# Performance work log

Hardware: AMD Instinct MI355X
Metric: run time of the kernel (lower is better)

The kernel has to match this reference:

```python
import jax, jax.numpy as jnp
import numpy as np

B, N, M, L = 4, 2048, 64, 64  # batch, targets, neighbors, lr_dim


def setup_inputs() -> dict:
    key = jax.random.key(0)
    ks = jax.random.split(key, 7)
    return {
        "targets_receptor": jax.random.normal(ks[0], (B, N, L), dtype=jnp.float32),
        "neighbors_ligand": jax.random.normal(ks[1], (B, N, M, L), dtype=jnp.float32),
        "a": jax.random.uniform(ks[2], (B, N, M), dtype=jnp.float32),
        "kernel_l": jax.random.normal(ks[3], (1, 1, L), dtype=jnp.float32),
        "bias_l": jax.random.normal(ks[4], (1, 1, L), dtype=jnp.float32),
        "kernel_r": jax.random.normal(ks[5], (1, 1, L), dtype=jnp.float32),
        "bias_r": jax.random.normal(ks[6], (1, 1, L), dtype=jnp.float32),
    }


def reference(targets_receptor, neighbors_ligand, a, kernel_l, bias_l, kernel_r, bias_r):
    # Per-feature affine transforms of receptor (targets) and ligand (neighbors).
    r = targets_receptor * kernel_r + bias_r                 # (B, N, L)
    lig = neighbors_ligand * kernel_l + bias_l               # (B, N, M, L)
    # weights[b,n,m,l] = r[b,n,l] * lig[b,n,m,l] * a[b,n,m]; sum over m.
    # Expressed as a fused einsum to avoid writing the (B,N,M,L) intermediate.
    w = jnp.einsum('bnl,bnml,bnm->bnl', r, lig, a)           # (B, N, L)
    return jax.nn.sigmoid(w)
```

## Files before the change

kernel.cpp:

```cpp
#include <hip/hip_runtime.h>
#include <math.h>


#define LDIM 64
#define MDIM 64

typedef float v4f __attribute__((ext_vector_type(4)));

__global__ __launch_bounds__(64) void slg_fused_kernel(
    const float* __restrict__ tr,
    const float* __restrict__ nl,
    const float* __restrict__ a,
    const float* __restrict__ kl,
    const float* __restrict__ bl,
    const float* __restrict__ kr,
    const float* __restrict__ br,
    float* __restrict__ out,
    int BN)
{
    const int bn = blockIdx.x;
    if (bn >= BN) return;
    const int lane = threadIdx.x & 63;

    const int colg = lane & 15;
    const int row0 = lane >> 4;
    const int l0 = colg * 4;

    const float* nlp = nl + (size_t)bn * (MDIM * LDIM);

    const float a_lane = a[(size_t)bn * MDIM + lane];
    const float4 t  = *reinterpret_cast<const float4*>(tr + (size_t)bn * LDIM + l0);
    const float4 K  = *reinterpret_cast<const float4*>(kl + l0);
    const float4 Bl = *reinterpret_cast<const float4*>(bl + l0);
    const float4 Kr = *reinterpret_cast<const float4*>(kr + l0);
    const float4 Br = *reinterpret_cast<const float4*>(br + l0);

    v4f v[16];
#pragma unroll
    for (int k = 0; k < 16; ++k)
        v[k] = __builtin_nontemporal_load(
            reinterpret_cast<const v4f*>(nlp + (row0 + 4 * k) * LDIM + l0));

    float am[16];
#pragma unroll
    for (int k = 0; k < 16; ++k)
        am[k] = __shfl(a_lane, row0 + 4 * k, 64);

    v4f acc = {0.f, 0.f, 0.f, 0.f};
#pragma unroll
    for (int k = 0; k < 16; ++k) {
        acc.x = fmaf(am[k], v[k].x, acc.x);
        acc.y = fmaf(am[k], v[k].y, acc.y);
        acc.z = fmaf(am[k], v[k].z, acc.z);
        acc.w = fmaf(am[k], v[k].w, acc.w);
    }

#pragma unroll
    for (int off = 16; off <= 32; off <<= 1) {
        acc.x += __shfl_xor(acc.x, off, 64);
        acc.y += __shfl_xor(acc.y, off, 64);
        acc.z += __shfl_xor(acc.z, off, 64);
        acc.w += __shfl_xor(acc.w, off, 64);
    }

    float asum = a_lane;
#pragma unroll
    for (int off = 1; off <= 32; off <<= 1)
        asum += __shfl_xor(asum, off, 64);

    float wx = (t.x * Kr.x + Br.x) * (K.x * acc.x + Bl.x * asum);
    float wy = (t.y * Kr.y + Br.y) * (K.y * acc.y + Bl.y * asum);
    float wz = (t.z * Kr.z + Br.z) * (K.z * acc.z + Bl.z * asum);
    float ww = (t.w * Kr.w + Br.w) * (K.w * acc.w + Bl.w * asum);

    v4f o;
    o.x = 1.0f / (1.0f + __expf(-wx));
    o.y = 1.0f / (1.0f + __expf(-wy));
    o.z = 1.0f / (1.0f + __expf(-wz));
    o.w = 1.0f / (1.0f + __expf(-ww));

    if (lane < 16) {
        __builtin_nontemporal_store(
            o, reinterpret_cast<v4f*>(out + (size_t)bn * LDIM + l0));
    }
}

extern "C" void kernel_launch(void* const* d_in, const int* in_sizes, int n_in,
                              void* d_out, int out_size, void* d_ws, size_t ws_size,
                              hipStream_t stream) {
    const float* tr = (const float*)d_in[0];
    const float* nl = (const float*)d_in[1];
    const float* a  = (const float*)d_in[2];
    const float* kl = (const float*)d_in[3];
    const float* bl = (const float*)d_in[4];
    const float* kr = (const float*)d_in[5];
    const float* br = (const float*)d_in[6];
    float* out = (float*)d_out;

    const int BN = in_sizes[0] / LDIM;
    const int block = 64;
    const int grid = BN;

    slg_fused_kernel<<<grid, block, 0, stream>>>(tr, nl, a, kl, bl, kr, br, out, BN);
}
```

Before: 193.5 us.

## Process multiple rows per wave with register double-buffered prefetch

Each 64-thread block now handles four (b,n) rows in a grid-stride pattern, prefetching the next row's 16 KB neighbor tile into a second register buffer while it reduces the current one. The goal is to hide global-memory latency inside a wave and to amortize the per-block loads of the kernel and bias vectors. The cost is more registers per thread and a grid four times smaller, which lowers the number of waves in flight available to hide latency.

```diff
diff --git a/kernel.cpp b/kernel.cpp
--- a/kernel.cpp
+++ b/kernel.cpp
@@ -4,55 +4,37 @@
 
 #define LDIM 64
 #define MDIM 64
+#define TPW  4
 
 typedef float v4f __attribute__((ext_vector_type(4)));
 
-__global__ __launch_bounds__(64) void slg_fused_kernel(
-    const float* __restrict__ tr,
-    const float* __restrict__ nl,
-    const float* __restrict__ a,
-    const float* __restrict__ kl,
-    const float* __restrict__ bl,
-    const float* __restrict__ kr,
-    const float* __restrict__ br,
-    float* __restrict__ out,
-    int BN)
+__device__ __forceinline__ void prefetch_tile(
+    const float* __restrict__ nl, const float* __restrict__ a,
+    const float* __restrict__ tr, int bn, int lane, int row0, int l0,
+    v4f (&v)[16], float& a_lane, float4& t)
 {
-    const int bn = blockIdx.x;
-    if (bn >= BN) return;
-    const int lane = threadIdx.x & 63;
-
-    const int colg = lane & 15;
-    const int row0 = lane >> 4;
-    const int l0 = colg * 4;
-
     const float* nlp = nl + (size_t)bn * (MDIM * LDIM);
-
-    const float a_lane = a[(size_t)bn * MDIM + lane];
-    const float4 t  = *reinterpret_cast<const float4*>(tr + (size_t)bn * LDIM + l0);
-    const float4 K  = *reinterpret_cast<const float4*>(kl + l0);
-    const float4 Bl = *reinterpret_cast<const float4*>(bl + l0);
-    const float4 Kr = *reinterpret_cast<const float4*>(kr + l0);
-    const float4 Br = *reinterpret_cast<const float4*>(br + l0);
-
-    v4f v[16];
+    a_lane = a[(size_t)bn * MDIM + lane];
+    t = *reinterpret_cast<const float4*>(tr + (size_t)bn * LDIM + l0);
 #pragma unroll
     for (int k = 0; k < 16; ++k)
         v[k] = __builtin_nontemporal_load(
             reinterpret_cast<const v4f*>(nlp + (row0 + 4 * k) * LDIM + l0));
+}
 
-    float am[16];
-#pragma unroll
-    for (int k = 0; k < 16; ++k)
-        am[k] = __shfl(a_lane, row0 + 4 * k, 64);
-
+__device__ __forceinline__ void compute_store_tile(
+    const v4f (&v)[16], float a_lane, const float4& t,
+    const float4& K, const float4& Bl, const float4& Kr, const float4& Br,
+    float* __restrict__ out, int bn, int lane, int row0, int l0)
+{
     v4f acc = {0.f, 0.f, 0.f, 0.f};
 #pragma unroll
     for (int k = 0; k < 16; ++k) {
-        acc.x = fmaf(am[k], v[k].x, acc.x);
-        acc.y = fmaf(am[k], v[k].y, acc.y);
-        acc.z = fmaf(am[k], v[k].z, acc.z);
-        acc.w = fmaf(am[k], v[k].w, acc.w);
+        const float am = __shfl(a_lane, row0 + 4 * k, 64);
+        acc.x = fmaf(am, v[k].x, acc.x);
+        acc.y = fmaf(am, v[k].y, acc.y);
+        acc.z = fmaf(am, v[k].z, acc.z);
+        acc.w = fmaf(am, v[k].w, acc.w);
     }
 
 #pragma unroll
@@ -68,10 +50,10 @@
     for (int off = 1; off <= 32; off <<= 1)
         asum += __shfl_xor(asum, off, 64);
 
-    float wx = (t.x * Kr.x + Br.x) * (K.x * acc.x + Bl.x * asum);
-    float wy = (t.y * Kr.y + Br.y) * (K.y * acc.y + Bl.y * asum);
-    float wz = (t.z * Kr.z + Br.z) * (K.z * acc.z + Bl.z * asum);
-    float ww = (t.w * Kr.w + Br.w) * (K.w * acc.w + Bl.w * asum);
+    const float wx = (t.x * Kr.x + Br.x) * (K.x * acc.x + Bl.x * asum);
+    const float wy = (t.y * Kr.y + Br.y) * (K.y * acc.y + Bl.y * asum);
+    const float wz = (t.z * Kr.z + Br.z) * (K.z * acc.z + Bl.z * asum);
+    const float ww = (t.w * Kr.w + Br.w) * (K.w * acc.w + Bl.w * asum);
 
     v4f o;
     o.x = 1.0f / (1.0f + __expf(-wx));
@@ -82,6 +64,54 @@
     if (lane < 16) {
         __builtin_nontemporal_store(
             o, reinterpret_cast<v4f*>(out + (size_t)bn * LDIM + l0));
+    }
+}
+
+__global__ __launch_bounds__(64) void slg_fused_kernel(
+    const float* __restrict__ tr,
+    const float* __restrict__ nl,
+    const float* __restrict__ a,
+    const float* __restrict__ kl,
+    const float* __restrict__ bl,
+    const float* __restrict__ kr,
+    const float* __restrict__ br,
+    float* __restrict__ out,
+    int BN)
+{
+    const int wid    = blockIdx.x;
+    const int stride = gridDim.x;
+    const int lane = threadIdx.x & 63;
+    const int colg = lane & 15;
+    const int row0 = lane >> 4;
+    const int l0 = colg * 4;
+
+    const float4 K  = *reinterpret_cast<const float4*>(kl + l0);
+    const float4 Bl = *reinterpret_cast<const float4*>(bl + l0);
+    const float4 Kr = *reinterpret_cast<const float4*>(kr + l0);
+    const float4 Br = *reinterpret_cast<const float4*>(br + l0);
+
+    v4f vA[16], vB[16];
+    float aA = 0.f, aB = 0.f;
+    float4 tA = {0,0,0,0}, tB = {0,0,0,0};
+
+    if (wid < BN)
+        prefetch_tile(nl, a, tr, wid, lane, row0, l0, vA, aA, tA);
+
+#pragma unroll
+    for (int t = 0; t < TPW; ++t) {
+        const int bn  = wid + t * stride;
+        const int bnn = bn + stride;
+        if ((t & 1) == 0) {
+            if (t + 1 < TPW && bnn < BN)
+                prefetch_tile(nl, a, tr, bnn, lane, row0, l0, vB, aB, tB);
+            if (bn < BN)
+                compute_store_tile(vA, aA, tA, K, Bl, Kr, Br, out, bn, lane, row0, l0);
+        } else {
+            if (t + 1 < TPW && bnn < BN)
+                prefetch_tile(nl, a, tr, bnn, lane, row0, l0, vA, aA, tA);
+            if (bn < BN)
+                compute_store_tile(vB, aB, tB, K, Bl, Kr, Br, out, bn, lane, row0, l0);
+        }
     }
 }
 
@@ -99,7 +129,7 @@
 
     const int BN = in_sizes[0] / LDIM;
     const int block = 64;
-    const int grid = BN;
+    const int grid = (BN + TPW - 1) / TPW;
 
     slg_fused_kernel<<<grid, block, 0, stream>>>(tr, nl, a, kl, bl, kr, br, out, BN);
 }
```

After: 193.6 us. No clear change (+0.0%).
